# Kernel optimization log

Measured on AMD Instinct MI355X. Metric: run time of the kernel, lower is better.

The kernel has to match this reference:

```python
import jax, jax.numpy as jnp
import numpy as np
from jax import lax

N, L, V, ES, HS = 16384, 512, 32000, 32, 64


def setup_inputs() -> dict:
    key = jax.random.key(0)
    k_tok, k_len, k_emb, k_wih, k_whh, k_bih, k_bhh = jax.random.split(key, 7)
    # valid tokens in [1, V) so that (x != 0).sum(1) == true prefix length
    tok = jax.random.randint(k_tok, (N, L), 1, V)
    lengths = jax.random.randint(k_len, (N,), 0, L + 1)  # includes empty seqs
    x = jnp.where(jnp.arange(L)[None, :] < lengths[:, None], tok, 0)
    s = 0.1
    embedding = jax.random.normal(k_emb, (V, ES), dtype=jnp.float32) * s
    w_ih = jax.random.normal(k_wih, (3 * HS, ES), dtype=jnp.float32) * s  # [r|z|n] stacked (torch order)
    w_hh = jax.random.normal(k_whh, (3 * HS, HS), dtype=jnp.float32) * s
    b_ih = jax.random.normal(k_bih, (3 * HS,), dtype=jnp.float32) * s
    b_hh = jax.random.normal(k_bhh, (3 * HS,), dtype=jnp.float32) * s
    return {"x": x, "embedding": embedding, "w_ih": w_ih, "w_hh": w_hh,
            "b_ih": b_ih, "b_hh": b_hh}


def reference(x, embedding, w_ih, w_hh, b_ih, b_hh):
    # Faithful math: final GRU hidden state over the nonzero prefix of each row;
    # rows with length 0 return zeros (h0). Equivalent to bucketed
    # pack_padded_sequence + GRU + scatter of final hidden states.
    n, l = x.shape
    hs = w_hh.shape[1]
    lengths = (x != 0).sum(axis=1)  # [n]

    def step(h, inp):
        t, xt = inp                      # xt: [n] token ids at time t
        e = embedding[xt]                # [n, es] gather
        gx = e @ w_ih.T + b_ih           # [n, 3*hs]
        gh = h @ w_hh.T + b_hh           # [n, 3*hs]
        xr, xz, xn = jnp.split(gx, 3, axis=-1)
        hr, hz, hn = jnp.split(gh, 3, axis=-1)
        r = jax.nn.sigmoid(xr + hr)
        z = jax.nn.sigmoid(xz + hz)
        ng = jnp.tanh(xn + r * hn)
        h_new = (1.0 - z) * ng + z * h   # torch GRU update
        h = jnp.where((t < lengths)[:, None], h_new, h)  # freeze past length
        return h, None

    h0 = jnp.zeros((n, hs), dtype=embedding.dtype)
    hT, _ = lax.scan(step, h0, (jnp.arange(l), x.T))
    return hT
```

## Files before the change

kernel.cpp:

```cpp
#include <hip/hip_runtime.h>

#define N_SEQ 16384
#define LSEQ  512
#define VOCAB 32000
#define ES    32
#define HS    64
#define LDH   72
#define TS    18

#define SC_RZ (-1.4426950408889634f)
#define SC_N  (-2.8853900817779268f)

typedef _Float16 v8h __attribute__((ext_vector_type(8)));
typedef float    v4f __attribute__((ext_vector_type(4)));
typedef float    v2f __attribute__((ext_vector_type(2)));

__global__ __launch_bounds__(256) void k_len(const int* __restrict__ x,
                                             int* __restrict__ len,
                                             int* __restrict__ hist){
  int row = blockIdx.x * 256 + threadIdx.x;
  const int* xr = x + (size_t)row * LSEQ;
  int lo = 0, hi = LSEQ;
  while (lo < hi){ int mid = (lo + hi) >> 1; if (xr[mid] != 0) lo = mid + 1; else hi = mid; }
  len[row] = lo;
  atomicAdd(&hist[lo], 1);
}

#define SCB   16
#define EMBV  125
__global__ __launch_bounds__(1024) void k_mid(const int* __restrict__ hist,
                                              const int* __restrict__ len,
                                              int* __restrict__ gcnt,
                                              int* __restrict__ perm,
                                              const float* __restrict__ emb,
                                              const float* __restrict__ whh,
                                              const float* __restrict__ wih,
                                              _Float16* __restrict__ ef,
                                              _Float16* __restrict__ wpk,
                                              _Float16* __restrict__ wpe){
  int b = blockIdx.x;
  if (b < SCB){
    __shared__ int buf[1024];
    __shared__ int offs[513];
    int i = threadIdx.x;
    buf[i] = (i < 513) ? hist[i] : 0;
    __syncthreads();
    for (int d = 1; d < 1024; d <<= 1){
      int v = (i >= d) ? buf[i - d] : 0;
      __syncthreads();
      buf[i] += v;
      __syncthreads();
    }
    if (i < 513) offs[i] = (i == 0) ? 0 : buf[i - 1];
    __syncthreads();
    int s = b * 1024 + i;
    int l = len[s];
    int pos = offs[l] + atomicAdd(&gcnt[l], 1);
    perm[pos] = s;
  } else if (b < SCB + EMBV){
    int i = ((b - SCB) * 1024 + threadIdx.x) * 8;
    float4 f0 = *(const float4*)(emb + i);
    float4 f1 = *(const float4*)(emb + i + 4);
    v8h o;
    o[0] = (_Float16)f0.x; o[1] = (_Float16)f0.y;
    o[2] = (_Float16)f0.z; o[3] = (_Float16)f0.w;
    o[4] = (_Float16)f1.x; o[5] = (_Float16)f1.y;
    o[6] = (_Float16)f1.z; o[7] = (_Float16)f1.w;
    *(v8h*)(ef + i) = o;
  } else {
    int tid = (b - SCB - EMBV) * 1024 + threadIdx.x;
    if (tid < 1536){
      int f = tid >> 6, l = tid & 63;
      int jt = f >> 1, kf = f & 1;
      float sc = (jt < 8) ? SC_RZ : SC_N;
      #pragma unroll
      for (int i = 0; i < 8; ++i){
        int row = jt * 16 + (l & 15);
        int col = kf * 32 + (l >> 4) * 8 + i;
        wpk[(size_t)tid * 8 + i] = (_Float16)(sc * whh[row * HS + col]);
      }
    } else if (tid < 1536 + 768){
      int t2 = tid - 1536;
      int tile = t2 >> 6, l = t2 & 63;
      float sc = ((tile >> 2) < 2) ? SC_RZ : SC_N;
      #pragma unroll
      for (int i = 0; i < 8; ++i){
        int row = tile * 16 + (l & 15);
        int col = (l >> 4) * 8 + i;
        wpe[(size_t)t2 * 8 + i] = (_Float16)(sc * wih[row * ES + col]);
      }
    }
  }
}

__global__ __launch_bounds__(256, 4) void k_gru(
    const int* __restrict__ x, const _Float16* __restrict__ ef,
    const _Float16* __restrict__ wpk, const _Float16* __restrict__ wpe,
    const float* __restrict__ bih, const float* __restrict__ bhh,
    const int* __restrict__ perm, const int* __restrict__ len,
    float* __restrict__ out)
{
  __shared__ __align__(16) _Float16 hb[2][16 * LDH];
  __shared__ unsigned short tok[(LSEQ + 2) * TS];
  int qt   = threadIdx.x >> 6;
  int w = blockIdx.x >> 8, cq = blockIdx.x & 255;
  int rank = w * 256 + ((w & 1) ? (255 - cq) : cq);
  int grp  = 1023 - rank;
  int lane = threadIdx.x & 63;
  int q = lane >> 4, c = lane & 15;
  int uu = qt*16 + c;

  v8h bfh[3][2], bfe[3];
  #pragma unroll
  for (int g = 0; g < 3; ++g){
    int tile = g*4 + qt;
    #pragma unroll
    for (int kf = 0; kf < 2; ++kf)
      bfh[g][kf] = *(const v8h*)(wpk + ((size_t)(tile*2 + kf)*64 + lane)*8);
    bfe[g] = *(const v8h*)(wpe + ((size_t)tile*64 + lane)*8);
  }

  int sq[4], ln[4];
  #pragma unroll
  for (int r = 0; r < 4; ++r){
    int s = perm[grp * 16 + q*4 + r];
    sq[r] = s;
    ln[r] = len[s];
  }
  float br  = SC_RZ * (bih[uu]      + bhh[uu]);
  float bz  = SC_RZ * (bih[HS + uu] + bhh[HS + uu]);
  float ben = SC_N  *  bih[2*HS + uu];
  float bhn = SC_N  *  bhh[2*HS + uu];
  v4f brq  = {br, br, br, br};
  v4f bzq  = {bz, bz, bz, bz};
  v4f benq = {ben, ben, ben, ben};
  v4f bhnq = {bhn, bhn, bhn, bhn};

  float h[4];
  #pragma unroll
  for (int r = 0; r < 4; ++r) h[r] = 0.f;

  for (int i = threadIdx.x; i < 16*LDH; i += 256) hb[0][i] = (_Float16)0.f;

  for (int j = threadIdx.x; j < 16*LSEQ; j += 256){
    int s = j >> 9, tt = j & (LSEQ-1);
    tok[tt*TS + s] = (unsigned short)x[(size_t)perm[grp*16 + s] * LSEQ + tt];
  }
  if (threadIdx.x < 32){
    tok[(LSEQ + (threadIdx.x >> 4))*TS + (threadIdx.x & 15)] = 0;
  }
  __syncthreads();

  int tmax = max(max(ln[0], ln[1]), max(ln[2], ln[3]));
  tmax = max(tmax, __shfl_xor(tmax, 16, 64));
  tmax = max(tmax, __shfl_xor(tmax, 32, 64));
  int tmin = min(min(ln[0], ln[1]), min(ln[2], ln[3]));
  tmin = min(tmin, __shfl_xor(tmin, 16, 64));
  tmin = min(tmin, __shfl_xor(tmin, 32, 64));

  v8h aec, aen;
  v4f pra, prb, pza, pzb, dea, deb;
  {
    int tk0 = tok[0*TS + c];
    aec = *(const v8h*)(ef + (size_t)tk0 * ES + q*8);
    pra = __builtin_amdgcn_mfma_f32_16x16x32_f16(aec, bfe[0], brq,  0,0,0);
    pza = __builtin_amdgcn_mfma_f32_16x16x32_f16(aec, bfe[1], bzq,  0,0,0);
    dea = __builtin_amdgcn_mfma_f32_16x16x32_f16(aec, bfe[2], benq, 0,0,0);
    int tk1 = tok[1*TS + c];
    aen = *(const v8h*)(ef + (size_t)tk1 * ES + q*8);
  }

  const v2f one2 = {1.f, 1.f};

  #define GRU_STEP(FREEZE, ACONS, ALOAD, PRR, PRZ, DEN, PRRn, PRZn, DENn, RB, WB) \
  {                                                                            \
    int tkn = tok[(t + 2)*TS + c];                                             \
    v8h a0 = *(const v8h*)(&hb[RB][c*LDH + q*8]);                              \
    v8h a1 = *(const v8h*)(&hb[RB][c*LDH + 32 + q*8]);                         \
    v4f zr  = __builtin_amdgcn_mfma_f32_16x16x32_f16(a1, bfh[0][1], PRR, 0,0,0);\
    v4f Dr  = __builtin_amdgcn_mfma_f32_16x16x32_f16(a0, bfh[0][0], zr,  0,0,0);\
    v4f zz  = __builtin_amdgcn_mfma_f32_16x16x32_f16(a1, bfh[1][1], PRZ, 0,0,0);\
    v4f Dz  = __builtin_amdgcn_mfma_f32_16x16x32_f16(a0, bfh[1][0], zz,  0,0,0);\
    v4f zh  = __builtin_amdgcn_mfma_f32_16x16x32_f16(a1, bfh[2][1], bhnq,0,0,0);\
    v4f Dhn = __builtin_amdgcn_mfma_f32_16x16x32_f16(a0, bfh[2][0], zh,  0,0,0);\
    _Pragma("unroll")                                                          \
    for (int p = 0; p < 2; ++p){                                               \
      v2f dr = {Dr[2*p],  Dr[2*p+1]};                                          \
      v2f dz = {Dz[2*p],  Dz[2*p+1]};                                          \
      v2f dn = {Dhn[2*p], Dhn[2*p+1]};                                         \
      v2f de = {DEN[2*p], DEN[2*p+1]};                                         \
      v2f hh = {h[2*p],   h[2*p+1]};                                           \
      v2f er, ez, rg, te, rd;                                                  \
      er[0] = __builtin_amdgcn_exp2f(dr[0]);                                   \
      er[1] = __builtin_amdgcn_exp2f(dr[1]);                                   \
      ez[0] = __builtin_amdgcn_exp2f(dz[0]);                                   \
      ez[1] = __builtin_amdgcn_exp2f(dz[1]);                                   \
      v2f ar = er + one2;                                                      \
      rg[0] = __builtin_amdgcn_rcpf(ar[0]);                                    \
      rg[1] = __builtin_amdgcn_rcpf(ar[1]);                                    \
      v2f ta = de + rg * dn;                                                   \
      te[0] = __builtin_amdgcn_exp2f(ta[0]);                                   \
      te[1] = __builtin_amdgcn_exp2f(ta[1]);                                   \
      v2f A   = te + one2;                                                     \
      v2f hp1 = hh + one2;                                                     \
      v2f e2  = ez + ez;                                                       \
      v2f num = A * hp1 + e2;                                                  \
      v2f den = A * (ez + one2);                                               \
      rd[0] = __builtin_amdgcn_rcpf(den[0]);                                   \
      rd[1] = __builtin_amdgcn_rcpf(den[1]);                                   \
      v2f hn2 = num * rd - one2;                                               \
      h[2*p]   = (FREEZE && t >= ln[2*p])   ? h[2*p]   : hn2[0];               \
      h[2*p+1] = (FREEZE && t >= ln[2*p+1]) ? h[2*p+1] : hn2[1];               \
    }                                                                          \
    PRRn = __builtin_amdgcn_mfma_f32_16x16x32_f16(ACONS, bfe[0], brq,  0,0,0); \
    PRZn = __builtin_amdgcn_mfma_f32_16x16x32_f16(ACONS, bfe[1], bzq,  0,0,0); \
    DENn = __builtin_amdgcn_mfma_f32_16x16x32_f16(ACONS, bfe[2], benq, 0,0,0); \
    ALOAD = *(const v8h*)(ef + (size_t)tkn * ES + q*8);           \
    _Pragma("unroll")                                                          \
    for (int r = 0; r < 4; ++r)                                                \
      hb[WB][(q*4 + r)*LDH + uu] = (_Float16)h[r];                             \
    asm volatile("s_waitcnt lgkmcnt(0)" ::: "memory");                         \
    __builtin_amdgcn_s_barrier();                                              \
    asm volatile("" ::: "memory");                                             \
  }

  int t = 0;
  for (; t + 1 < tmin; ){
    GRU_STEP(0, aen, aec, pra, pza, dea, prb, pzb, deb, 0, 1); ++t;
    GRU_STEP(0, aec, aen, prb, pzb, deb, pra, pza, dea, 1, 0); ++t;
  }
  for (; t + 1 < tmax; ){
    GRU_STEP(1, aen, aec, pra, pza, dea, prb, pzb, deb, 0, 1); ++t;
    GRU_STEP(1, aec, aen, prb, pzb, deb, pra, pza, dea, 1, 0); ++t;
  }
  if (t < tmax){
    GRU_STEP(1, aen, aec, pra, pza, dea, prb, pzb, deb, 0, 1); ++t;
  }
  #undef GRU_STEP

  #pragma unroll
  for (int r = 0; r < 4; ++r)
    out[(size_t)sq[r] * HS + uu] = h[r];
}

extern "C" void kernel_launch(void* const* d_in, const int* in_sizes, int n_in,
                              void* d_out, int out_size, void* d_ws, size_t ws_size,
                              hipStream_t stream){
  const int*   x   = (const int*)  d_in[0];
  const float* emb = (const float*)d_in[1];
  const float* wih = (const float*)d_in[2];
  const float* whh = (const float*)d_in[3];
  const float* bih = (const float*)d_in[4];
  const float* bhh = (const float*)d_in[5];
  float* out = (float*)d_out;

  char* ws = (char*)d_ws;
  size_t off = 0;
  _Float16* ef  = (_Float16*)(ws + off);  off += (size_t)VOCAB * ES * sizeof(_Float16);
  _Float16* wpk = (_Float16*)(ws + off);  off += (size_t)24 * 64 * 8 * sizeof(_Float16);
  _Float16* wpe = (_Float16*)(ws + off);  off += (size_t)12 * 64 * 8 * sizeof(_Float16);
  off = (off + 255) & ~(size_t)255;
  int* len  = (int*)(ws + off);           off += (size_t)N_SEQ * sizeof(int);
  int* perm = (int*)(ws + off);           off += (size_t)N_SEQ * sizeof(int);
  int* hist = (int*)(ws + off);           off += 513 * sizeof(int);
  int* gcnt = (int*)(ws + off);           off += 513 * sizeof(int);

  hipMemsetAsync(hist, 0, 2 * 513 * sizeof(int), stream);
  k_len <<<N_SEQ / 256, 256, 0, stream>>>(x, len, hist);
  k_mid <<<SCB + EMBV + 3, 1024, 0, stream>>>(hist, len, gcnt, perm,
                                              emb, whh, wih, ef, wpk, wpe);
  k_gru <<<N_SEQ / 16,    256, 0, stream>>>(x, ef, wpk, wpe, bih, bhh, perm, len, out);
}
```

Measured before the change: 311.6 us.

## Concatenate longest and shortest sorted sequences per lane to balance recurrence lengths

Each MFMA row slot now processes two sequences back to back: one from the long end of the length-sorted permutation and one from the short end. The hidden state is written out and reset to zero at the boundary. The grid is halved and every block's step count approaches the sum of a paired long and short length, which evens out the tail imbalance. The token buffer doubles to 1024 steps, occupancy drops to two blocks per CU, and the gate math is rewritten in scalar form. The added branch at every step and the larger LDS use are the cost.

```diff
diff --git a/kernel.cpp b/kernel.cpp
--- a/kernel.cpp
+++ b/kernel.cpp
@@ -7,13 +7,15 @@
 #define HS    64
 #define LDH   72
 #define TS    18
+#define RT    1024
+#define NCH   (N_SEQ / 2)
+#define NBLK  (NCH / 16)
 
 #define SC_RZ (-1.4426950408889634f)
 #define SC_N  (-2.8853900817779268f)
 
 typedef _Float16 v8h __attribute__((ext_vector_type(8)));
 typedef float    v4f __attribute__((ext_vector_type(4)));
-typedef float    v2f __attribute__((ext_vector_type(2)));
 
 __global__ __launch_bounds__(256) void k_len(const int* __restrict__ x,
                                              int* __restrict__ len,
@@ -93,7 +95,7 @@
   }
 }
 
-__global__ __launch_bounds__(256, 4) void k_gru(
+__global__ __launch_bounds__(256, 2) void k_gru(
     const int* __restrict__ x, const _Float16* __restrict__ ef,
     const _Float16* __restrict__ wpk, const _Float16* __restrict__ wpe,
     const float* __restrict__ bih, const float* __restrict__ bhh,
@@ -101,11 +103,10 @@
     float* __restrict__ out)
 {
   __shared__ __align__(16) _Float16 hb[2][16 * LDH];
-  __shared__ unsigned short tok[(LSEQ + 2) * TS];
+  __shared__ unsigned short tok[RT * TS];
+  __shared__ int sA[16], sB[16], sLA[16], sLB[16];
   int qt   = threadIdx.x >> 6;
-  int w = blockIdx.x >> 8, cq = blockIdx.x & 255;
-  int rank = w * 256 + ((w & 1) ? (255 - cq) : cq);
-  int grp  = 1023 - rank;
+  int grp  = blockIdx.x;
   int lane = threadIdx.x & 63;
   int q = lane >> 4, c = lane & 15;
   int uu = qt*16 + c;
@@ -120,13 +121,24 @@
     bfe[g] = *(const v8h*)(wpe + ((size_t)tile*64 + lane)*8);
   }
 
-  int sq[4], ln[4];
+  if (threadIdx.x < 16){
+    int ch = grp*16 + threadIdx.x;
+    int a  = perm[(N_SEQ - 1) - ch];
+    int b2 = perm[ch];
+    sA[threadIdx.x] = a;  sB[threadIdx.x] = b2;
+    sLA[threadIdx.x] = len[a]; sLB[threadIdx.x] = len[b2];
+  }
+  for (int i = threadIdx.x; i < 16*LDH; i += 256) hb[0][i] = (_Float16)0.f;
+  __syncthreads();
+
+  int sqA[4], sqB[4], lnA[4], lnT[4];
   #pragma unroll
   for (int r = 0; r < 4; ++r){
-    int s = perm[grp * 16 + q*4 + r];
-    sq[r] = s;
-    ln[r] = len[s];
-  }
+    int s0 = q*4 + r;
+    sqA[r] = sA[s0];  sqB[r] = sB[s0];
+    lnA[r] = sLA[s0]; lnT[r] = sLA[s0] + sLB[s0];
+  }
+
   float br  = SC_RZ * (bih[uu]      + bhh[uu]);
   float bz  = SC_RZ * (bih[HS + uu] + bhh[HS + uu]);
   float ben = SC_N  *  bih[2*HS + uu];
@@ -140,21 +152,21 @@
   #pragma unroll
   for (int r = 0; r < 4; ++r) h[r] = 0.f;
 
-  for (int i = threadIdx.x; i < 16*LDH; i += 256) hb[0][i] = (_Float16)0.f;
-
-  for (int j = threadIdx.x; j < 16*LSEQ; j += 256){
-    int s = j >> 9, tt = j & (LSEQ-1);
-    tok[tt*TS + s] = (unsigned short)x[(size_t)perm[grp*16 + s] * LSEQ + tt];
-  }
-  if (threadIdx.x < 32){
-    tok[(LSEQ + (threadIdx.x >> 4))*TS + (threadIdx.x & 15)] = 0;
+  for (int j = threadIdx.x; j < 16*RT; j += 256){
+    int s = j >> 10, tt = j & (RT-1);
+    int la  = sLA[s];
+    int isA = tt < la;
+    int tb  = tt - la; tb = tb < 511 ? tb : 511;
+    int seq = isA ? sA[s] : sB[s];
+    int tc  = isA ? tt : tb;
+    tok[tt*TS + s] = (unsigned short)x[(size_t)seq * LSEQ + tc];
   }
   __syncthreads();
 
-  int tmax = max(max(ln[0], ln[1]), max(ln[2], ln[3]));
+  int tmax = max(max(lnT[0], lnT[1]), max(lnT[2], lnT[3]));
   tmax = max(tmax, __shfl_xor(tmax, 16, 64));
   tmax = max(tmax, __shfl_xor(tmax, 32, 64));
-  int tmin = min(min(ln[0], ln[1]), min(ln[2], ln[3]));
+  int tmin = min(min(lnT[0], lnT[1]), min(lnT[2], lnT[3]));
   tmin = min(tmin, __shfl_xor(tmin, 16, 64));
   tmin = min(tmin, __shfl_xor(tmin, 32, 64));
 
@@ -170,11 +182,9 @@
     aen = *(const v8h*)(ef + (size_t)tk1 * ES + q*8);
   }
 
-  const v2f one2 = {1.f, 1.f};
-
   #define GRU_STEP(FREEZE, ACONS, ALOAD, PRR, PRZ, DEN, PRRn, PRZn, DENn, RB, WB) \
   {                                                                            \
-    int tkn = tok[(t + 2)*TS + c];                                             \
+    int tkn = tok[((t + 2) & (RT-1))*TS + c];                                  \
     v8h a0 = *(const v8h*)(&hb[RB][c*LDH + q*8]);                              \
     v8h a1 = *(const v8h*)(&hb[RB][c*LDH + 32 + q*8]);                         \
     v4f zr  = __builtin_amdgcn_mfma_f32_16x16x32_f16(a1, bfh[0][1], PRR, 0,0,0);\
@@ -184,33 +194,23 @@
     v4f zh  = __builtin_amdgcn_mfma_f32_16x16x32_f16(a1, bfh[2][1], bhnq,0,0,0);\
     v4f Dhn = __builtin_amdgcn_mfma_f32_16x16x32_f16(a0, bfh[2][0], zh,  0,0,0);\
     _Pragma("unroll")                                                          \
-    for (int p = 0; p < 2; ++p){                                               \
-      v2f dr = {Dr[2*p],  Dr[2*p+1]};                                          \
-      v2f dz = {Dz[2*p],  Dz[2*p+1]};                                          \
-      v2f dn = {Dhn[2*p], Dhn[2*p+1]};                                         \
-      v2f de = {DEN[2*p], DEN[2*p+1]};                                         \
-      v2f hh = {h[2*p],   h[2*p+1]};                                           \
-      v2f er, ez, rg, te, rd;                                                  \
-      er[0] = __builtin_amdgcn_exp2f(dr[0]);                                   \
-      er[1] = __builtin_amdgcn_exp2f(dr[1]);                                   \
-      ez[0] = __builtin_amdgcn_exp2f(dz[0]);                                   \
-      ez[1] = __builtin_amdgcn_exp2f(dz[1]);                                   \
-      v2f ar = er + one2;                                                      \
-      rg[0] = __builtin_amdgcn_rcpf(ar[0]);                                    \
-      rg[1] = __builtin_amdgcn_rcpf(ar[1]);                                    \
-      v2f ta = de + rg * dn;                                                   \
-      te[0] = __builtin_amdgcn_exp2f(ta[0]);                                   \
-      te[1] = __builtin_amdgcn_exp2f(ta[1]);                                   \
-      v2f A   = te + one2;                                                     \
-      v2f hp1 = hh + one2;                                                     \
-      v2f e2  = ez + ez;                                                       \
-      v2f num = A * hp1 + e2;                                                  \
-      v2f den = A * (ez + one2);                                               \
-      rd[0] = __builtin_amdgcn_rcpf(den[0]);                                   \
-      rd[1] = __builtin_amdgcn_rcpf(den[1]);                                   \
-      v2f hn2 = num * rd - one2;                                               \
-      h[2*p]   = (FREEZE && t >= ln[2*p])   ? h[2*p]   : hn2[0];               \
-      h[2*p+1] = (FREEZE && t >= ln[2*p+1]) ? h[2*p+1] : hn2[1];               \
+    for (int r = 0; r < 4; ++r){                                               \
+      float rg   = __builtin_amdgcn_rcpf(1.f + __builtin_amdgcn_exp2f(Dr[r])); \
+      float zg   = __builtin_amdgcn_rcpf(1.f + __builtin_amdgcn_exp2f(Dz[r])); \
+      float te   = __builtin_amdgcn_exp2f(DEN[r] + rg * Dhn[r]);               \
+      float ng   = fmaf(2.f, __builtin_amdgcn_rcpf(1.f + te), -1.f);           \
+      float hnew = ng + zg * (h[r] - ng);                                      \
+      h[r]       = (FREEZE && t >= lnT[r]) ? h[r] : hnew;                      \
+    }                                                                          \
+    {                                                                          \
+      int f0 = (t + 1 == lnA[0]), f1 = (t + 1 == lnA[1]);                      \
+      int f2 = (t + 1 == lnA[2]), f3 = (t + 1 == lnA[3]);                      \
+      if (f0 | f1 | f2 | f3){                                                  \
+        if (f0){ out[(size_t)sqA[0]*HS + uu] = h[0]; h[0] = 0.f; }             \
+        if (f1){ out[(size_t)sqA[1]*HS + uu] = h[1]; h[1] = 0.f; }             \
+        if (f2){ out[(size_t)sqA[2]*HS + uu] = h[2]; h[2] = 0.f; }             \
+        if (f3){ out[(size_t)sqA[3]*HS + uu] = h[3]; h[3] = 0.f; }             \
+      }                                                                        \
     }                                                                          \
     PRRn = __builtin_amdgcn_mfma_f32_16x16x32_f16(ACONS, bfe[0], brq,  0,0,0); \
     PRZn = __builtin_amdgcn_mfma_f32_16x16x32_f16(ACONS, bfe[1], bzq,  0,0,0); \
@@ -239,8 +239,10 @@
   #undef GRU_STEP
 
   #pragma unroll
-  for (int r = 0; r < 4; ++r)
-    out[(size_t)sq[r] * HS + uu] = h[r];
+  for (int r = 0; r < 4; ++r){
+    out[(size_t)sqB[r]*HS + uu] = h[r];
+    if (lnA[r] == 0) out[(size_t)sqA[r]*HS + uu] = 0.f;
+  }
 }
 
 extern "C" void kernel_launch(void* const* d_in, const int* in_sizes, int n_in,
@@ -269,5 +271,5 @@
   k_len <<<N_SEQ / 256, 256, 0, stream>>>(x, len, hist);
   k_mid <<<SCB + EMBV + 3, 1024, 0, stream>>>(hist, len, gcnt, perm,
                                               emb, whh, wih, ef, wpk, wpe);
-  k_gru <<<N_SEQ / 16,    256, 0, stream>>>(x, ef, wpk, wpe, bih, bhh, perm, len, out);
-}
+  k_gru <<<NBLK, 256, 0, stream>>>(x, ef, wpk, wpe, bih, bhh, perm, len, out);
+}
```

Result: slower. 354.5 us (+13.8%).
